# Optimization experiments

Measured on AMD Instinct MI355X. Metric: run time of the kernel, lower is better.

## Reference

```python
import jax, jax.numpy as jnp
import numpy as np

B, A = 8192, 16
HID, NK, NQ, NV = 256, 32, 32, 128
IN_DIM, CUR_HID, CUR_OUT, N_ACT = 512, 512, 128, 64
EXT_LAMBD, INT_LAMBD = 1.0, 0.5


def setup_inputs() -> dict:
    key = jax.random.key(0)
    ks = jax.random.split(key, 16)
    def w(k, i, o):
        return jax.random.normal(k, (i, o), jnp.float32) / np.sqrt(i)
    return {
        'x': jax.random.normal(ks[0], (B * A, IN_DIM), jnp.float32),
        'hidden': jax.random.normal(ks[1], (B, A, HID), jnp.float32),
        'Wk': w(ks[2], HID, NK), 'bk': jnp.zeros((NK,), jnp.float32),
        'Wv': w(ks[3], HID, NV), 'bv': jnp.zeros((NV,), jnp.float32),
        'Wq': w(ks[4], HID, NQ), 'bq': jnp.zeros((NQ,), jnp.float32),
        'Wa': w(ks[5], NQ + NK * A, A), 'ba': jnp.zeros((A,), jnp.float32),
        'Wt1': w(ks[6], IN_DIM, CUR_HID), 'bt1': jnp.zeros((CUR_HID,), jnp.float32),
        'Wt2': w(ks[7], CUR_HID, CUR_OUT), 'bt2': jnp.zeros((CUR_OUT,), jnp.float32),
        'Wp1': w(ks[8], IN_DIM, CUR_HID), 'bp1': jnp.zeros((CUR_HID,), jnp.float32),
        'Wp2': w(ks[9], CUR_HID, CUR_HID), 'bp2': jnp.zeros((CUR_HID,), jnp.float32),
        'Wp3': w(ks[10], CUR_HID, CUR_OUT), 'bp3': jnp.zeros((CUR_OUT,), jnp.float32),
        'Wc': w(ks[11], NV + HID, HID), 'bc': jnp.zeros((HID,), jnp.float32),
        'W2': w(ks[12], HID, N_ACT), 'b2': jnp.zeros((N_ACT,), jnp.float32),
    }


def _aggregate(x, hidden, Wk, bk, Wv, bv, Wq, bq, Wa, ba, Wt1, bt1, Wt2, bt2,
               Wp1, bp1, Wp2, bp2, Wp3, bp3, Wc, bc, W2, b2):
    # communicate(): per-agent key / value / query projections
    key_ = hidden @ Wk + bk          # [B, A, NK]
    value = hidden @ Wv + bv         # [B, A, NV]
    query = hidden @ Wq + bq         # [B, A, NQ]
    # torch.cat([key[:, i, :] for i in range(A)], -1) == reshape; repeat == broadcast
    flat_key = key_.reshape(B, A * NK)
    qk = jnp.concatenate(
        [query, jnp.broadcast_to(flat_key[:, None, :], (B, A, A * NK))], axis=-1)
    attn_weights = jax.nn.softmax(qk @ Wa + ba, axis=-1)   # [B, A, A]
    # intrinsic-motivation predictors (dropout p=0.5 in eval mode -> identity)
    tar = jax.nn.relu(x @ Wt1 + bt1) @ Wt2 + bt2           # [B*A, CUR_OUT]
    pred = jax.nn.relu(x @ Wp1 + bp1)
    pred = jax.nn.relu(pred @ Wp2 + bp2)
    pred = pred @ Wp3 + bp3
    int_imp = jnp.mean((tar - pred) ** 2, axis=-1).reshape(B, A)
    int_imp = jax.nn.softmax(int_imp, axis=-1)             # [B, A]
    # view(B,A,1).repeat(1,1,A).permute(0,2,1): out[b,i,j] = int_imp[b,j]
    int_mat = jnp.broadcast_to(int_imp[:, None, :], (B, A, A))
    attn = EXT_LAMBD * attn_weights + INT_LAMBD * jax.lax.stop_gradient(int_mat)
    applied = jnp.einsum('bij,bjv->biv', attn, value)      # [B, A, NV]
    comb = jax.nn.relu(jnp.concatenate([applied, hidden], axis=-1) @ Wc + bc)
    return comb @ W2 + b2                                  # [B, A, N_ACT]


def reference(x, hidden, Wk, bk, Wv, bv, Wq, bq, Wa, ba, Wt1, bt1, Wt2, bt2,
              Wp1, bp1, Wp2, bp2, Wp3, bp3, Wc, bc, W2, b2):
    return _aggregate(x, hidden, Wk, bk, Wv, bv, Wq, bq, Wa, ba, Wt1, bt1,
                      Wt2, bt2, Wp1, bp1, Wp2, bp2, Wp3, bp3, Wc, bc, W2, b2)
```

## Files before the change

### kernel.cpp

```cpp
#include <hip/hip_runtime.h>
#include <cstddef>
#include <cstdint>

typedef unsigned short ushort_t;
typedef __attribute__((ext_vector_type(4))) float f32x4;
typedef __attribute__((ext_vector_type(8))) short bf16x8;

#define BB   8192
#define AA   16
#define BA   131072

__device__ __forceinline__ float bf2f(ushort_t u) {
    union { float f; uint32_t i; } v; v.i = ((uint32_t)u) << 16; return v.f;
}
__device__ __forceinline__ ushort_t f2bf(float f) {
    union { float f; uint32_t i; } v; v.f = f;
    uint32_t r = v.i + 0x7fffu + ((v.i >> 16) & 1u);
    return (ushort_t)(r >> 16);
}
__device__ __forceinline__ void gload_lds16(const void* g, void* l) {
    __builtin_amdgcn_global_load_lds(
        (const __attribute__((address_space(1))) uint32_t*)g,
        (__attribute__((address_space(3))) uint32_t*)l, 16, 0, 0);
}

template<bool RELU, bool FUSE_OUT>
__global__ __launch_bounds__(512, 2)
void gemm8p(const ushort_t* __restrict__ A, int lda,
            const ushort_t* __restrict__ A2, int lda2, int ksplit,
            const ushort_t* __restrict__ Bt,
            const float* __restrict__ bias,
            ushort_t* __restrict__ C, int ldc, int K, int lgx, int rpx,
            const ushort_t* __restrict__ W2t, const float* __restrict__ b2)
{
    __shared__ ushort_t lds[65536];

    const int tid  = threadIdx.x;
    const int w    = tid >> 6;
    const int lane = tid & 63;
    const int wm   = w >> 2;
    const int wn   = w & 3;
    const int fr   = lane & 15;
    const int fq   = lane >> 4;

    const int bid  = blockIdx.x;
    const int xcd  = bid & 7;
    const int slot = bid >> 3;
    const int x    = slot & ((1 << lgx) - 1);
    const int y    = xcd * rpx + (slot >> lgx);
    const size_t brow = (size_t)y * 256;
    const int    bcol = x * 256;

    const int NT = K >> 6;
    const int NI = NT >> 1;

    const int srl = tid >> 3;
    const int spg = tid & 7;

    f32x4 acc[8][4];
#pragma unroll
    for (int m = 0; m < 8; ++m)
#pragma unroll
        for (int n = 0; n < 4; ++n) acc[m][n] = (f32x4){0.f, 0.f, 0.f, 0.f};

    const ushort_t* aB1[4];
    const ushort_t* aB2[4];
    const ushort_t* bB[4];
    int ldsA[4], ldsB[4];
#pragma unroll
    for (int s = 0; s < 4; ++s) {
        const int rowA = (srl < 32) ? s * 32 + srl : 128 + s * 32 + (srl - 32);
        const int colA = ((spg ^ (rowA & 7)) << 3);
        aB1[s] = A  + (brow + rowA) * (size_t)lda  + colA;
        aB2[s] = A2 + (brow + rowA) * (size_t)lda2 + colA - ksplit;
        ldsA[s] = rowA * 64 + spg * 8;
        const int rowB = s * 64 + srl;
        const int colB = ((spg ^ (rowB & 7)) << 3);
        bB[s]   = Bt + (size_t)(bcol + rowB) * K + colB;
        ldsB[s] = 16384 + rowB * 64 + spg * 8;
    }

    auto stageA = [&](int T, int s, int bi) {
        const int k0 = T << 6;
        const ushort_t* src = (k0 >= ksplit ? aB2[s] : aB1[s]) + k0;
        gload_lds16(src, &lds[(bi << 15) + ldsA[s]]);
    };
    auto stageB = [&](int T, int c, int bi) {
        gload_lds16(bB[c] + (T << 6), &lds[(bi << 15) + ldsB[c]]);
    };

    stageA(0, 0, 0); stageB(0, 0, 0);
    stageA(0, 1, 0); stageB(0, 1, 0);
    stageA(0, 2, 0); stageB(0, 2, 0);
    stageA(0, 3, 0); stageB(0, 3, 0);
    stageA(1, 0, 1); stageB(1, 0, 1);
    stageA(1, 1, 1); stageB(1, 1, 1);
    stageA(1, 2, 1); stageB(1, 2, 1);

    bf16x8 breg[4][2];

    for (int i = 0; i < NI; ++i) {
        const bool more = (i + 1 < NI);
#pragma unroll
        for (int h = 0; h < 2; ++h) {
            const int bufA = h << 15;
            const int bufB = (h << 15) + 16384;
#pragma unroll
            for (int q = 0; q < 4; ++q) {
                if (q == 0) {
                    if (h == 0 || more) asm volatile("s_waitcnt vmcnt(6)" ::: "memory");
                    else                asm volatile("s_waitcnt vmcnt(0)" ::: "memory");
                    __builtin_amdgcn_sched_barrier(0);
                    __builtin_amdgcn_s_barrier();
#pragma unroll
                    for (int n = 0; n < 4; ++n)
#pragma unroll
                        for (int kk = 0; kk < 2; ++kk) {
                            const int row = wn * 64 + n * 16 + fr;
                            const int gp  = ((kk * 4 + fq) ^ (row & 7)) << 3;
                            breg[n][kk] = *(const bf16x8*)&lds[bufB + row * 64 + gp];
                        }
                }
                bf16x8 areg[2][2];
#pragma unroll
                for (int j = 0; j < 2; ++j)
#pragma unroll
                    for (int kk = 0; kk < 2; ++kk) {
                        const int row = wm * 128 + (2 * q + j) * 16 + fr;
                        const int gp  = ((kk * 4 + fq) ^ (row & 7)) << 3;
                        areg[j][kk] = *(const bf16x8*)&lds[bufA + row * 64 + gp];
                    }
                if (h == 0) {
                    if (q == 0)      { stageA(2*i+1, 3, 1); stageB(2*i+1, 3, 1); }
                    else if (more)   { stageA(2*i+2, q-1, 0); stageB(2*i+2, q-1, 0); }
                } else {
                    if (q == 0) { if (more) { stageA(2*i+2, 3, 0); stageB(2*i+2, 3, 0); } }
                    else        { if (more) { stageA(2*i+3, q-1, 1); stageB(2*i+3, q-1, 1); } }
                }
                __builtin_amdgcn_s_setprio(1);
#pragma unroll
                for (int j = 0; j < 2; ++j)
#pragma unroll
                    for (int n = 0; n < 4; ++n)
#pragma unroll
                        for (int kk = 0; kk < 2; ++kk)
                            acc[2*q+j][n] = __builtin_amdgcn_mfma_f32_16x16x32_bf16(
                                areg[j][kk], breg[n][kk], acc[2*q+j][n], 0, 0, 0);
                __builtin_amdgcn_s_setprio(0);
                __builtin_amdgcn_s_barrier();
            }
        }
    }

    if (!FUSE_OUT) {
#pragma unroll
        for (int m = 0; m < 8; ++m) {
            const size_t rowb = brow + wm * 128 + m * 16 + fq * 4;
#pragma unroll
            for (int n = 0; n < 4; ++n) {
                const int col = bcol + wn * 64 + n * 16 + fr;
                const float bv = bias[col];
#pragma unroll
                for (int r = 0; r < 4; ++r) {
                    float v = acc[m][n][r] + bv;
                    if (RELU) v = fmaxf(v, 0.f);
                    C[(rowb + r) * (size_t)ldc + col] = f2bf(v);
                }
            }
        }
    } else {
#pragma unroll
        for (int m = 0; m < 8; ++m) {
            const int row = wm * 128 + m * 16 + fq * 4;
#pragma unroll
            for (int n = 0; n < 4; ++n) {
                const int col = wn * 64 + n * 16 + fr;
                const float bv = bias[col];
#pragma unroll
                for (int r = 0; r < 4; ++r) {
                    const float v = fmaxf(acc[m][n][r] + bv, 0.f);
                    const int rr = row + r;
                    const int g  = (col >> 3) ^ (rr & 7);
                    lds[rr * 256 + g * 8 + (col & 7)] = f2bf(v);
                }
            }
        }
        bf16x8 w2f[4][8];
#pragma unroll
        for (int n2 = 0; n2 < 4; ++n2)
#pragma unroll
            for (int kk = 0; kk < 8; ++kk)
                w2f[n2][kk] = *(const bf16x8*)&W2t[(n2 * 16 + fr) * 256 + kk * 32 + fq * 8];
        __syncthreads();
        f32x4 acc2[2][4];
#pragma unroll
        for (int m2 = 0; m2 < 2; ++m2)
#pragma unroll
            for (int n2 = 0; n2 < 4; ++n2) acc2[m2][n2] = (f32x4){0.f, 0.f, 0.f, 0.f};
#pragma unroll
        for (int kk = 0; kk < 8; ++kk) {
#pragma unroll
            for (int m2 = 0; m2 < 2; ++m2) {
                const int row = w * 32 + m2 * 16 + fr;
                const int g   = (kk * 4 + fq) ^ (row & 7);
                const bf16x8 af = *(const bf16x8*)&lds[row * 256 + g * 8];
#pragma unroll
                for (int n2 = 0; n2 < 4; ++n2)
                    acc2[m2][n2] = __builtin_amdgcn_mfma_f32_16x16x32_bf16(
                        af, w2f[n2][kk], acc2[m2][n2], 0, 0, 0);
            }
        }
        float* outp = (float*)C;
#pragma unroll
        for (int m2 = 0; m2 < 2; ++m2) {
            const size_t rowb = brow + w * 32 + m2 * 16 + fq * 4;
#pragma unroll
            for (int n2 = 0; n2 < 4; ++n2) {
                const int col = n2 * 16 + fr;
                const float bv = b2[col];
#pragma unroll
                for (int r = 0; r < 4; ++r)
                    outp[(rowb + r) * 64 + col] = acc2[m2][n2][r] + bv;
            }
        }
    }
}

template<bool OBF16, bool RELU, bool MSE>
__global__ __launch_bounds__(256)
void gemm_mfma(const ushort_t* __restrict__ A, int lda,
               const ushort_t* __restrict__ A2, int lda2, int ksplit,
               const ushort_t* __restrict__ Bt,
               const float* __restrict__ bias,
               void* __restrict__ C, int ldc, int N, int K, int lgx,
               float* __restrict__ iimp_out)
{
    __shared__ ushort_t As[2][128 * 64];
    __shared__ ushort_t Bs[2][128 * 64];

    const int tid  = threadIdx.x;
    const int w    = tid >> 6;
    const int lane = tid & 63;
    const int wm   = w >> 1;
    const int wn   = w & 1;

    const int bid  = blockIdx.x;
    const int xcd  = bid & 7;
    const int slot = bid >> 3;
    const int x    = slot & ((1 << lgx) - 1);
    const int y    = xcd * 128 + (slot >> lgx);
    const size_t brow = (size_t)y * 128;
    const int    bcol = x * 128;

    const int fr   = lane & 15;
    const int fq   = lane >> 4;
    const int srow = lane >> 3;
    const int scol = (lane & 7) << 3;

    f32x4 acc[4][4];
#pragma unroll
    for (int i = 0; i < 4; ++i)
#pragma unroll
        for (int j = 0; j < 4; ++j) acc[i][j] = (f32x4){0.f, 0.f, 0.f, 0.f};

    const int NT = K >> 6;

    auto stage = [&](int buf, int k0) {
#pragma unroll
        for (int i = 0; i < 4; ++i) {
            const int c = (w << 2) + i;
            const int r = (c << 3) + srow;
            const ushort_t* asrc;
            if (k0 >= ksplit)
                asrc = A2 + (brow + r) * (size_t)lda2 + (k0 - ksplit) + scol;
            else
                asrc = A  + (brow + r) * (size_t)lda  + k0 + scol;
            gload_lds16(asrc, &As[buf][(c << 9) + lane * 8]);
            gload_lds16(Bt + (size_t)(bcol + r) * K + k0 + scol,
                        &Bs[buf][(c << 9) + lane * 8]);
        }
    };

    stage(0, 0);
    __syncthreads();

    for (int t = 0; t < NT; ++t) {
        const int cur = t & 1;
        if (t + 1 < NT) stage(cur ^ 1, (t + 1) << 6);
#pragma unroll
        for (int kk = 0; kk < 2; ++kk) {
            bf16x8 a[4], b[4];
#pragma unroll
            for (int f = 0; f < 4; ++f) {
                a[f] = *(const bf16x8*)&As[cur][(wm * 64 + f * 16 + fr) * 64 + kk * 32 + fq * 8];
                b[f] = *(const bf16x8*)&Bs[cur][(wn * 64 + f * 16 + fr) * 64 + kk * 32 + fq * 8];
            }
#pragma unroll
            for (int fm = 0; fm < 4; ++fm)
#pragma unroll
                for (int fn = 0; fn < 4; ++fn)
                    acc[fm][fn] = __builtin_amdgcn_mfma_f32_16x16x32_bf16(
                        a[fm], b[fn], acc[fm][fn], 0, 0, 0);
        }
        __syncthreads();
    }

    if (MSE) {
        float* rowsq = (float*)As;
        if (tid < 128) rowsq[tid] = 0.f;
        __syncthreads();
#pragma unroll
        for (int fm = 0; fm < 4; ++fm) {
#pragma unroll
            for (int r = 0; r < 4; ++r) {
                float s = 0.f;
#pragma unroll
                for (int fn = 0; fn < 4; ++fn) {
                    const int col = wn * 64 + fn * 16 + fr;
                    const float v = acc[fm][fn][r] + bias[col];
                    s += v * v;
                }
                s += __shfl_xor(s, 1);
                s += __shfl_xor(s, 2);
                s += __shfl_xor(s, 4);
                s += __shfl_xor(s, 8);
                if (fr == 0)
                    atomicAdd(&rowsq[wm * 64 + fm * 16 + fq * 4 + r], s);
            }
        }
        __syncthreads();
        if (tid < 8) {
            const int rb = tid * 16;
            float mv[16], mx = -1e30f;
#pragma unroll
            for (int a = 0; a < 16; ++a) {
                mv[a] = rowsq[rb + a] * (1.f / 128.f);
                mx = fmaxf(mx, mv[a]);
            }
            float e[16], den = 0.f;
#pragma unroll
            for (int a = 0; a < 16; ++a) { e[a] = __expf(mv[a] - mx); den += e[a]; }
            const float inv = 1.f / den;
            const size_t b = brow / 16 + tid;
#pragma unroll
            for (int a = 0; a < 16; ++a) iimp_out[b * 16 + a] = e[a] * inv;
        }
        return;
    }

#pragma unroll
    for (int fm = 0; fm < 4; ++fm) {
        const size_t rowb = brow + wm * 64 + fm * 16 + fq * 4;
#pragma unroll
        for (int fn = 0; fn < 4; ++fn) {
            const int col = bcol + wn * 64 + fn * 16 + fr;
            if (col < N) {
                const float bv = bias[col];
#pragma unroll
                for (int r = 0; r < 4; ++r) {
                    float v = acc[fm][fn][r] + bv;
                    if (RELU) v = fmaxf(v, 0.f);
                    const size_t idx = (rowb + r) * (size_t)ldc + col;
                    if (OBF16) ((ushort_t*)C)[idx] = f2bf(v);
                    else       ((float*)C)[idx]    = v;
                }
            }
        }
    }
}

__global__ __launch_bounds__(256)
void transpose_w(const float* __restrict__ W, ushort_t* __restrict__ Wt,
                 int K, int N, int Npad)
{
    int idx = blockIdx.x * 256 + threadIdx.x;
    if (idx >= Npad * K) return;
    int n = idx / K, k = idx - n * K;
    float v = (n < N) ? W[(size_t)k * N + n] : 0.f;
    Wt[idx] = f2bf(v);
}

__global__ __launch_bounds__(256)
void transpose_wk(const float* __restrict__ W, ushort_t* __restrict__ Wt,
                  int Ksrc, int N, int ldk, int kOff, float sign)
{
    int idx = blockIdx.x * 256 + threadIdx.x;
    if (idx >= N * Ksrc) return;
    int n = idx / Ksrc, k = idx - n * Ksrc;
    Wt[(size_t)n * ldk + kOff + k] = f2bf(sign * W[(size_t)k * N + n]);
}

__global__ __launch_bounds__(256)
void conv_f32_bf16(const float* __restrict__ src, ushort_t* __restrict__ dst)
{
    size_t q = (size_t)blockIdx.x * 256 + threadIdx.x;
    float4 v = ((const float4*)src)[q];
    ushort_t* d = dst + q * 4;
    d[0] = f2bf(v.x); d[1] = f2bf(v.y); d[2] = f2bf(v.z); d[3] = f2bf(v.w);
}

__global__ void pack_cat2(const float* __restrict__ a, const float* __restrict__ b,
                          float* __restrict__ o)
{
    int j = blockIdx.x * 256 + threadIdx.x;
    if (j < 512) o[j] = a[j];
    else if (j < 1024) o[j] = b[j - 512];
}

__global__ void pack_bias(const float* __restrict__ bk, const float* __restrict__ bq,
                          const float* __restrict__ bv, float* __restrict__ pb)
{
    int j = threadIdx.x;
    float v = 0.f;
    if      (j < 32)  v = bk[j];
    else if (j < 64)  v = bq[j - 32];
    else if (j < 192) v = bv[j - 64];
    pb[j] = v;
}

__global__ void make_cbias(const float* __restrict__ bt2, const float* __restrict__ bp3,
                           float* __restrict__ cb)
{
    int j = threadIdx.x;
    cb[j] = bt2[j] - bp3[j];
}

__global__ __launch_bounds__(256)
void attn_apply(const ushort_t* __restrict__ kvq, const float* __restrict__ Wa,
                const float* __restrict__ ba, const float* __restrict__ iimp,
                ushort_t* __restrict__ applied)
{
    const int b = blockIdx.x, t = threadIdx.x;
    __shared__ float klds[512], qlds[512];
    __shared__ ushort_t vlds[2048];
    __shared__ float part[16][17];
    __shared__ float kp[16];
    __shared__ float attn[16][17];

    for (int i = t; i < 512; i += 256) {
        int a = i >> 5, c = i & 31;
        const size_t base = ((size_t)b * AA + a) * 192;
        klds[i] = bf2f(kvq[base + c]);
        qlds[i] = bf2f(kvq[base + 32 + c]);
    }
    for (int i = t; i < 2048; i += 256) {
        int j = i >> 7, v = i & 127;
        vlds[i] = kvq[((size_t)b * AA + j) * 192 + 64 + v];
    }
    __syncthreads();

    {
        int j = t & 15, seg = t >> 4;
        float s = 0.f;
        for (int c = seg * 32; c < seg * 32 + 32; ++c)
            s += klds[c] * Wa[(32 + c) * 16 + j];
        part[j][seg] = s;
    }
    __syncthreads();
    if (t < 16) {
        float s = 0.f;
#pragma unroll
        for (int seg = 0; seg < 16; ++seg) s += part[t][seg];
        kp[t] = s;
    }
    __syncthreads();

    {
        int i = t >> 4, j = t & 15;
        float s = 0.f;
#pragma unroll
        for (int q = 0; q < 32; ++q) s += qlds[i * 32 + q] * Wa[q * 16 + j];
        attn[i][j] = s + kp[j] + ba[j];
    }
    __syncthreads();
    if (t < 16) {
        float mx = -1e30f;
#pragma unroll
        for (int j = 0; j < 16; ++j) mx = fmaxf(mx, attn[t][j]);
        float e[16], den = 0.f;
#pragma unroll
        for (int j = 0; j < 16; ++j) { e[j] = __expf(attn[t][j] - mx); den += e[j]; }
        float inv = 1.f / den;
#pragma unroll
        for (int j = 0; j < 16; ++j)
            attn[t][j] = e[j] * inv + 0.5f * iimp[b * 16 + j];
    }
    __syncthreads();

    for (int o = t; o < 2048; o += 256) {
        int i = o >> 7, v = o & 127;
        float s = 0.f;
#pragma unroll
        for (int j = 0; j < 16; ++j) s += attn[i][j] * bf2f(vlds[j * 128 + v]);
        applied[((size_t)b * AA + i) * 128 + v] = f2bf(s);
    }
}

extern "C" void kernel_launch(void* const* d_in, const int* in_sizes, int n_in,
                              void* d_out, int out_size, void* d_ws, size_t ws_size,
                              hipStream_t stream)
{
    const float* x      = (const float*)d_in[0];
    const float* hidden = (const float*)d_in[1];
    const float* Wk  = (const float*)d_in[2];
    const float* bk  = (const float*)d_in[3];
    const float* Wv  = (const float*)d_in[4];
    const float* bv  = (const float*)d_in[5];
    const float* Wq  = (const float*)d_in[6];
    const float* bq  = (const float*)d_in[7];
    const float* Wa  = (const float*)d_in[8];
    const float* ba  = (const float*)d_in[9];
    const float* Wt1 = (const float*)d_in[10];
    const float* bt1 = (const float*)d_in[11];
    const float* Wt2 = (const float*)d_in[12];
    const float* bt2 = (const float*)d_in[13];
    const float* Wp1 = (const float*)d_in[14];
    const float* bp1 = (const float*)d_in[15];
    const float* Wp2 = (const float*)d_in[16];
    const float* bp2 = (const float*)d_in[17];
    const float* Wp3 = (const float*)d_in[18];
    const float* bp3 = (const float*)d_in[19];
    const float* Wc  = (const float*)d_in[20];
    const float* bc  = (const float*)d_in[21];
    const float* W2  = (const float*)d_in[22];
    const float* b2  = (const float*)d_in[23];

    float*    out = (float*)d_out;
    ushort_t* ws  = (ushort_t*)d_ws;

    ushort_t* xb  = ws;
    ushort_t* ht2 = xb + (size_t)BA * 512;
    ushort_t* hp2 = ht2 + (size_t)BA * 1024;
    ushort_t* WT  = hp2 + (size_t)BA * 512;
    ushort_t* kvq     = xb;
    ushort_t* hiddenb = hp2;
    ushort_t* applied = ht2;

    ushort_t* Bg1  = WT;
    ushort_t* Wp2t = Bg1  + 1024 * 512;
    ushort_t* Dt   = Wp2t + 512 * 512;
    ushort_t* Wkvq = Dt   + 128 * 1024;
    ushort_t* Wct  = Wkvq + 256 * 256;
    ushort_t* W2t  = Wct  + 256 * 384;
    float* g1bias = (float*)(W2t + 128 * 256);
    float* pbias  = g1bias + 1024;
    float* cbias  = pbias + 256;
    float* iimp   = cbias + 128;

    const dim3 blk(256);
    const int BIG = 1 << 30;

    transpose_w<<<1024, blk, 0, stream>>>(Wt1, Bg1,             512, 512, 512);
    transpose_w<<<1024, blk, 0, stream>>>(Wp1, Bg1 + 512 * 512, 512, 512, 512);
    transpose_w<<<1024, blk, 0, stream>>>(Wp2, Wp2t, 512, 512, 512);
    transpose_wk<<<256, blk, 0, stream>>>(Wt2, Dt, 512, 128, 1024, 0,    1.f);
    transpose_wk<<<256, blk, 0, stream>>>(Wp3, Dt, 512, 128, 1024, 512, -1.f);
    transpose_w<<<32,  blk, 0, stream>>>(Wk, Wkvq + 0 * 256,   256, 32, 32);
    transpose_w<<<32,  blk, 0, stream>>>(Wq, Wkvq + 32 * 256,  256, 32, 32);
    transpose_w<<<128, blk, 0, stream>>>(Wv, Wkvq + 64 * 256,  256, 128, 128);
    transpose_w<<<64,  blk, 0, stream>>>(Wk, Wkvq + 192 * 256, 256, 0, 64);
    transpose_w<<<384, blk, 0, stream>>>(Wc, Wct, 384, 256, 256);
    transpose_w<<<128, blk, 0, stream>>>(W2, W2t, 256, 64, 128);
    pack_cat2<<<4, 256, 0, stream>>>(bt1, bp1, g1bias);
    pack_bias<<<1, 256, 0, stream>>>(bk, bq, bv, pbias);
    make_cbias<<<1, 128, 0, stream>>>(bt2, bp3, cbias);

    conv_f32_bf16<<<65536, blk, 0, stream>>>(x, xb);
    gemm8p<true, false><<<2048, 512, 0, stream>>>(
        xb, 512, xb, 512, BIG, Bg1, g1bias, ht2, 1024, 512, 2, 64, nullptr, nullptr);
    gemm8p<true, false><<<1024, 512, 0, stream>>>(
        ht2 + 512, 1024, ht2 + 512, 1024, BIG, Wp2t, bp2, hp2, 512, 512, 1, 64, nullptr, nullptr);
    gemm_mfma<true, false, true><<<1024, blk, 0, stream>>>(
        ht2, 1024, hp2, 512, 512, Dt, cbias, nullptr, 128, 128, 1024, 0, iimp);

    conv_f32_bf16<<<32768, blk, 0, stream>>>(hidden, hiddenb);
    gemm_mfma<true, false, false><<<2048, blk, 0, stream>>>(
        hiddenb, 256, hiddenb, 256, BIG, Wkvq, pbias, kvq, 192, 192, 256, 1, nullptr);
    attn_apply<<<BB, blk, 0, stream>>>(kvq, Wa, ba, iimp, applied);

    gemm8p<true, true><<<512, 512, 0, stream>>>(
        applied, 128, hiddenb, 256, 128, Wct, bc, (ushort_t*)out, 64, 384, 0, 64, W2t, b2);
}
```

Measured before the change: 599.7 us.

## Run curiosity predictor MLP GEMMs in FP8 e4m3 instead of bf16

Converts x and the curiosity-network weights (Wt1, Wp1, Wp2, Wt2, Wp3) to FP8 e4m3. It adds new FP8 MFMA GEMM kernels, including a swizzled-LDS 256x256 tile version and an FP8 MSE+softmax reduction kernel, and the intermediate activations are stored as FP8. The aim is to halve memory traffic and double matrix throughput for the dominant 131072x512 GEMMs. The risk is accuracy: intermediate activations and the tar-pred difference are quantized to 3-bit mantissa with no scaling. The attention and output paths stay in bf16, and the workspace layout is reorganized to fit.

```diff
diff --git a/kernel.cpp b/kernel.cpp
--- a/kernel.cpp
+++ b/kernel.cpp
@@ -3,6 +3,7 @@
 #include <cstdint>
 
 typedef unsigned short ushort_t;
+typedef unsigned char  u8_t;
 typedef __attribute__((ext_vector_type(4))) float f32x4;
 typedef __attribute__((ext_vector_type(8))) short bf16x8;
 
@@ -18,10 +19,274 @@
     uint32_t r = v.i + 0x7fffu + ((v.i >> 16) & 1u);
     return (ushort_t)(r >> 16);
 }
+__device__ __forceinline__ u8_t f2e4m3(float f) {
+    union { float f; uint32_t u; } v; v.f = f;
+    uint32_t s = (v.u >> 24) & 0x80u;
+    float a = fabsf(f);
+    if (a >= 448.f) return (u8_t)(s | 0x7Eu);
+    union { float f; uint32_t u; } w; w.f = a;
+    int E = (int)(w.u >> 23) - 127;
+    if (E < -6) E = -6;
+    union { uint32_t u; float f; } qs; qs.u = (uint32_t)(127 + 3 - E) << 23;
+    int m = (int)rintf(a * qs.f);
+    if (m >= 16) { m >>= 1; ++E; if (E > 8) return (u8_t)(s | 0x7Eu); }
+    if (m >= 8)  return (u8_t)(s | ((uint32_t)(E + 7) << 3) | (uint32_t)(m - 8));
+    return (u8_t)(s | (uint32_t)m);
+}
 __device__ __forceinline__ void gload_lds16(const void* g, void* l) {
     __builtin_amdgcn_global_load_lds(
         (const __attribute__((address_space(1))) uint32_t*)g,
         (__attribute__((address_space(3))) uint32_t*)l, 16, 0, 0);
+}
+
+template<bool RELU>
+__global__ __launch_bounds__(512, 2)
+void gemm8p_fp8(const u8_t* __restrict__ A, int lda,
+                const u8_t* __restrict__ A2, int lda2, int ksplit,
+                const u8_t* __restrict__ Bt,
+                const float* __restrict__ bias,
+                u8_t* __restrict__ C, int ldc, int K, int lgx, int rpx)
+{
+    __shared__ u8_t lds[65536];
+
+    const int tid  = threadIdx.x;
+    const int w    = tid >> 6;
+    const int lane = tid & 63;
+    const int wm   = w >> 2;
+    const int wn   = w & 3;
+    const int fr   = lane & 15;
+    const int fq   = lane >> 4;
+
+    const int bid  = blockIdx.x;
+    const int xcd  = bid & 7;
+    const int slot = bid >> 3;
+    const int x    = slot & ((1 << lgx) - 1);
+    const int y    = xcd * rpx + (slot >> lgx);
+    const size_t brow = (size_t)y * 256;
+    const int    bcol = x * 256;
+
+    const int NT = K >> 6;
+
+    f32x4 acc[8][4];
+#pragma unroll
+    for (int m = 0; m < 8; ++m)
+#pragma unroll
+        for (int n = 0; n < 4; ++n) acc[m][n] = (f32x4){0.f, 0.f, 0.f, 0.f};
+
+    size_t aoff[2], a2off[2], boff[2];
+    int aldso[2], bldso[2];
+#pragma unroll
+    for (int j = 0; j < 2; ++j) {
+        const int r = tid + (j << 9);
+        const int l = r >> 3;
+        const int p = r & 7;
+        const int g = p ^ (l & 7);
+        const int row  = 2 * l + (g >> 2);
+        const int colb = (g & 3) * 16;
+        aoff[j]  = (brow + row) * (size_t)lda  + colb;
+        a2off[j] = (brow + row) * (size_t)lda2 + colb;
+        boff[j]  = (size_t)(bcol + row) * K + colb;
+        aldso[j] = r * 16;
+        bldso[j] = 16384 + r * 16;
+    }
+
+    auto stage_tile = [&](int T) {
+        const int k0   = T << 6;
+        const int base = (T & 1) << 15;
+        const bool hi  = (k0 >= ksplit);
+#pragma unroll
+        for (int j = 0; j < 2; ++j) {
+            const u8_t* src = hi ? (A2 + a2off[j] + (k0 - ksplit))
+                                 : (A  + aoff[j]  + k0);
+            gload_lds16(src, &lds[base + aldso[j]]);
+        }
+#pragma unroll
+        for (int j = 0; j < 2; ++j)
+            gload_lds16(Bt + boff[j] + k0, &lds[base + bldso[j]]);
+    };
+
+    stage_tile(0);
+
+    unsigned long breg[4][2];
+
+    for (int t = 0; t < NT; ++t) {
+        const int base = (t & 1) << 15;
+#pragma unroll
+        for (int q = 0; q < 4; ++q) {
+            if (q == 0) {
+                asm volatile("s_waitcnt vmcnt(0)" ::: "memory");
+                __builtin_amdgcn_sched_barrier(0);
+                __builtin_amdgcn_s_barrier();
+#pragma unroll
+                for (int n = 0; n < 4; ++n)
+#pragma unroll
+                    for (int kk = 0; kk < 2; ++kk) {
+                        const int row  = wn * 64 + n * 16 + fr;
+                        const int l    = row >> 1;
+                        const int slotq = kk * 2 + (fq >> 1);
+                        const int g    = (row & 1) * 4 + slotq;
+                        const int p    = g ^ (l & 7);
+                        const int addr = base + 16384 + l * 128 + p * 16 + (fq & 1) * 8;
+                        breg[n][kk] = *(const unsigned long*)&lds[addr];
+                    }
+                if (t + 1 < NT) stage_tile(t + 1);
+            }
+            unsigned long areg[2][2];
+#pragma unroll
+            for (int j = 0; j < 2; ++j)
+#pragma unroll
+                for (int kk = 0; kk < 2; ++kk) {
+                    const int row  = wm * 128 + (2 * q + j) * 16 + fr;
+                    const int l    = row >> 1;
+                    const int slotq = kk * 2 + (fq >> 1);
+                    const int g    = (row & 1) * 4 + slotq;
+                    const int p    = g ^ (l & 7);
+                    const int addr = base + l * 128 + p * 16 + (fq & 1) * 8;
+                    areg[j][kk] = *(const unsigned long*)&lds[addr];
+                }
+            __builtin_amdgcn_s_setprio(1);
+#pragma unroll
+            for (int j = 0; j < 2; ++j)
+#pragma unroll
+                for (int n = 0; n < 4; ++n)
+#pragma unroll
+                    for (int kk = 0; kk < 2; ++kk)
+                        acc[2*q+j][n] = __builtin_amdgcn_mfma_f32_16x16x32_fp8_fp8(
+                            (long)areg[j][kk], (long)breg[n][kk], acc[2*q+j][n], 0, 0, 0);
+            __builtin_amdgcn_s_setprio(0);
+            __builtin_amdgcn_s_barrier();
+        }
+    }
+
+#pragma unroll
+    for (int m = 0; m < 8; ++m) {
+        const size_t rowb = brow + wm * 128 + m * 16 + fq * 4;
+#pragma unroll
+        for (int n = 0; n < 4; ++n) {
+            const int col = bcol + wn * 64 + n * 16 + fr;
+            const float bv = bias[col];
+#pragma unroll
+            for (int r = 0; r < 4; ++r) {
+                float v = acc[m][n][r] + bv;
+                if (RELU) v = fmaxf(v, 0.f);
+                C[(rowb + r) * (size_t)ldc + col] = f2e4m3(v);
+            }
+        }
+    }
+}
+
+__global__ __launch_bounds__(256)
+void gemm_mfma_fp8_mse(const u8_t* __restrict__ A, int lda,
+                       const u8_t* __restrict__ A2, int lda2, int ksplit,
+                       const u8_t* __restrict__ Bt,
+                       const float* __restrict__ bias,
+                       int K, float* __restrict__ iimp_out)
+{
+    __shared__ u8_t As[2][8192];
+    __shared__ u8_t Bs[2][8192];
+
+    const int tid  = threadIdx.x;
+    const int w    = tid >> 6;
+    const int lane = tid & 63;
+    const int wm   = w >> 1;
+    const int wn   = w & 1;
+
+    const int bid  = blockIdx.x;
+    const int xcd  = bid & 7;
+    const int slot = bid >> 3;
+    const int y    = xcd * 128 + slot;
+    const size_t brow = (size_t)y * 128;
+
+    const int fr = lane & 15;
+    const int fq = lane >> 4;
+
+    f32x4 acc[4][4];
+#pragma unroll
+    for (int i = 0; i < 4; ++i)
+#pragma unroll
+        for (int j = 0; j < 4; ++j) acc[i][j] = (f32x4){0.f, 0.f, 0.f, 0.f};
+
+    const int NT = K >> 6;
+
+    auto stage = [&](int buf, int k0) {
+#pragma unroll
+        for (int j = 0; j < 2; ++j) {
+            const int gi  = tid + (j << 8);
+            const int row = gi >> 2;
+            const int cb  = (gi & 3) * 16;
+            const u8_t* asrc;
+            if (k0 >= ksplit)
+                asrc = A2 + (brow + row) * (size_t)lda2 + (k0 - ksplit) + cb;
+            else
+                asrc = A  + (brow + row) * (size_t)lda  + k0 + cb;
+            gload_lds16(asrc, &As[buf][gi * 16]);
+            gload_lds16(Bt + (size_t)row * K + k0 + cb, &Bs[buf][gi * 16]);
+        }
+    };
+
+    stage(0, 0);
+    __syncthreads();
+
+    for (int t = 0; t < NT; ++t) {
+        const int cur = t & 1;
+        if (t + 1 < NT) stage(cur ^ 1, (t + 1) << 6);
+#pragma unroll
+        for (int kk = 0; kk < 2; ++kk) {
+            unsigned long a[4], b[4];
+#pragma unroll
+            for (int f = 0; f < 4; ++f) {
+                a[f] = *(const unsigned long*)&As[cur][(wm * 64 + f * 16 + fr) * 64 + kk * 32 + fq * 8];
+                b[f] = *(const unsigned long*)&Bs[cur][(wn * 64 + f * 16 + fr) * 64 + kk * 32 + fq * 8];
+            }
+#pragma unroll
+            for (int fm = 0; fm < 4; ++fm)
+#pragma unroll
+                for (int fn = 0; fn < 4; ++fn)
+                    acc[fm][fn] = __builtin_amdgcn_mfma_f32_16x16x32_fp8_fp8(
+                        (long)a[fm], (long)b[fn], acc[fm][fn], 0, 0, 0);
+        }
+        __syncthreads();
+    }
+
+    float* rowsq = (float*)As;
+    if (tid < 128) rowsq[tid] = 0.f;
+    __syncthreads();
+#pragma unroll
+    for (int fm = 0; fm < 4; ++fm) {
+#pragma unroll
+        for (int r = 0; r < 4; ++r) {
+            float s = 0.f;
+#pragma unroll
+            for (int fn = 0; fn < 4; ++fn) {
+                const int col = wn * 64 + fn * 16 + fr;
+                const float v = acc[fm][fn][r] + bias[col];
+                s += v * v;
+            }
+            s += __shfl_xor(s, 1);
+            s += __shfl_xor(s, 2);
+            s += __shfl_xor(s, 4);
+            s += __shfl_xor(s, 8);
+            if (fr == 0)
+                atomicAdd(&rowsq[wm * 64 + fm * 16 + fq * 4 + r], s);
+        }
+    }
+    __syncthreads();
+    if (tid < 8) {
+        const int rb = tid * 16;
+        float mv[16], mx = -1e30f;
+#pragma unroll
+        for (int a = 0; a < 16; ++a) {
+            mv[a] = rowsq[rb + a] * (1.f / 128.f);
+            mx = fmaxf(mx, mv[a]);
+        }
+        float e[16], den = 0.f;
+#pragma unroll
+        for (int a = 0; a < 16; ++a) { e[a] = __expf(mv[a] - mx); den += e[a]; }
+        const float inv = 1.f / den;
+        const size_t b = brow / 16 + tid;
+#pragma unroll
+        for (int a = 0; a < 16; ++a) iimp_out[b * 16 + a] = e[a] * inv;
+    }
 }
 
 template<bool RELU, bool FUSE_OUT>
@@ -226,14 +491,11 @@
     }
 }
 
-template<bool OBF16, bool RELU, bool MSE>
 __global__ __launch_bounds__(256)
 void gemm_mfma(const ushort_t* __restrict__ A, int lda,
-               const ushort_t* __restrict__ A2, int lda2, int ksplit,
                const ushort_t* __restrict__ Bt,
                const float* __restrict__ bias,
-               void* __restrict__ C, int ldc, int N, int K, int lgx,
-               float* __restrict__ iimp_out)
+               ushort_t* __restrict__ C, int ldc, int N, int K, int lgx)
 {
     __shared__ ushort_t As[2][128 * 64];
     __shared__ ushort_t Bs[2][128 * 64];
@@ -270,12 +532,8 @@
         for (int i = 0; i < 4; ++i) {
             const int c = (w << 2) + i;
             const int r = (c << 3) + srow;
-            const ushort_t* asrc;
-            if (k0 >= ksplit)
-                asrc = A2 + (brow + r) * (size_t)lda2 + (k0 - ksplit) + scol;
-            else
-                asrc = A  + (brow + r) * (size_t)lda  + k0 + scol;
-            gload_lds16(asrc, &As[buf][(c << 9) + lane * 8]);
+            gload_lds16(A + (brow + r) * (size_t)lda + k0 + scol,
+                        &As[buf][(c << 9) + lane * 8]);
             gload_lds16(Bt + (size_t)(bcol + r) * K + k0 + scol,
                         &Bs[buf][(c << 9) + lane * 8]);
         }
@@ -303,49 +561,6 @@
                         a[fm], b[fn], acc[fm][fn], 0, 0, 0);
         }
         __syncthreads();
-    }
-
-    if (MSE) {
-        float* rowsq = (float*)As;
-        if (tid < 128) rowsq[tid] = 0.f;
-        __syncthreads();
-#pragma unroll
-        for (int fm = 0; fm < 4; ++fm) {
-#pragma unroll
-            for (int r = 0; r < 4; ++r) {
-                float s = 0.f;
-#pragma unroll
-                for (int fn = 0; fn < 4; ++fn) {
-                    const int col = wn * 64 + fn * 16 + fr;
-                    const float v = acc[fm][fn][r] + bias[col];
-                    s += v * v;
-                }
-                s += __shfl_xor(s, 1);
-                s += __shfl_xor(s, 2);
-                s += __shfl_xor(s, 4);
-                s += __shfl_xor(s, 8);
-                if (fr == 0)
-                    atomicAdd(&rowsq[wm * 64 + fm * 16 + fq * 4 + r], s);
-            }
-        }
-        __syncthreads();
-        if (tid < 8) {
-            const int rb = tid * 16;
-            float mv[16], mx = -1e30f;
-#pragma unroll
-            for (int a = 0; a < 16; ++a) {
-                mv[a] = rowsq[rb + a] * (1.f / 128.f);
-                mx = fmaxf(mx, mv[a]);
-            }
-            float e[16], den = 0.f;
-#pragma unroll
-            for (int a = 0; a < 16; ++a) { e[a] = __expf(mv[a] - mx); den += e[a]; }
-            const float inv = 1.f / den;
-            const size_t b = brow / 16 + tid;
-#pragma unroll
-            for (int a = 0; a < 16; ++a) iimp_out[b * 16 + a] = e[a] * inv;
-        }
-        return;
     }
 
 #pragma unroll
@@ -357,13 +572,8 @@
             if (col < N) {
                 const float bv = bias[col];
 #pragma unroll
-                for (int r = 0; r < 4; ++r) {
-                    float v = acc[fm][fn][r] + bv;
-                    if (RELU) v = fmaxf(v, 0.f);
-                    const size_t idx = (rowb + r) * (size_t)ldc + col;
-                    if (OBF16) ((ushort_t*)C)[idx] = f2bf(v);
-                    else       ((float*)C)[idx]    = v;
-                }
+                for (int r = 0; r < 4; ++r)
+                    C[(rowb + r) * (size_t)ldc + col] = f2bf(acc[fm][fn][r] + bv);
             }
         }
     }
@@ -381,13 +591,24 @@
 }
 
 __global__ __launch_bounds__(256)
-void transpose_wk(const float* __restrict__ W, ushort_t* __restrict__ Wt,
-                  int Ksrc, int N, int ldk, int kOff, float sign)
+void transpose_w_fp8(const float* __restrict__ W, u8_t* __restrict__ Wt,
+                     int K, int N, int Npad)
+{
+    int idx = blockIdx.x * 256 + threadIdx.x;
+    if (idx >= Npad * K) return;
+    int n = idx / K, k = idx - n * K;
+    float v = (n < N) ? W[(size_t)k * N + n] : 0.f;
+    Wt[idx] = f2e4m3(v);
+}
+
+__global__ __launch_bounds__(256)
+void transpose_wk_fp8(const float* __restrict__ W, u8_t* __restrict__ Wt,
+                      int Ksrc, int N, int ldk, int kOff, float sign)
 {
     int idx = blockIdx.x * 256 + threadIdx.x;
     if (idx >= N * Ksrc) return;
     int n = idx / Ksrc, k = idx - n * Ksrc;
-    Wt[(size_t)n * ldk + kOff + k] = f2bf(sign * W[(size_t)k * N + n]);
+    Wt[(size_t)n * ldk + kOff + k] = f2e4m3(sign * W[(size_t)k * N + n]);
 }
 
 __global__ __launch_bounds__(256)
@@ -397,6 +618,16 @@
     float4 v = ((const float4*)src)[q];
     ushort_t* d = dst + q * 4;
     d[0] = f2bf(v.x); d[1] = f2bf(v.y); d[2] = f2bf(v.z); d[3] = f2bf(v.w);
+}
+
+__global__ __launch_bounds__(256)
+void conv_f32_fp8(const float* __restrict__ src, u8_t* __restrict__ dst)
+{
+    size_t q = (size_t)blockIdx.x * 256 + threadIdx.x;
+    float4 v = ((const float4*)src)[q];
+    uint32_t pk = (uint32_t)f2e4m3(v.x) | ((uint32_t)f2e4m3(v.y) << 8) |
+                  ((uint32_t)f2e4m3(v.z) << 16) | ((uint32_t)f2e4m3(v.w) << 24);
+    ((uint32_t*)dst)[q] = pk;
 }
 
 __global__ void pack_cat2(const float* __restrict__ a, const float* __restrict__ b,
@@ -525,21 +756,21 @@
     const float* W2  = (const float*)d_in[22];
     const float* b2  = (const float*)d_in[23];
 
-    float*    out = (float*)d_out;
-    ushort_t* ws  = (ushort_t*)d_ws;
-
-    ushort_t* xb  = ws;
-    ushort_t* ht2 = xb + (size_t)BA * 512;
-    ushort_t* hp2 = ht2 + (size_t)BA * 1024;
-    ushort_t* WT  = hp2 + (size_t)BA * 512;
-    ushort_t* kvq     = xb;
-    ushort_t* hiddenb = hp2;
-    ushort_t* applied = ht2;
-
-    ushort_t* Bg1  = WT;
-    ushort_t* Wp2t = Bg1  + 1024 * 512;
-    ushort_t* Dt   = Wp2t + 512 * 512;
-    ushort_t* Wkvq = Dt   + 128 * 1024;
+    float* out = (float*)d_out;
+    u8_t*  ws8 = (u8_t*)d_ws;
+
+    u8_t* xb8 = ws8;
+    u8_t* ht8 = xb8 + (size_t)BA * 512;
+    u8_t* hp8 = ht8 + (size_t)BA * 1024;
+    u8_t* WT  = hp8 + (size_t)BA * 512;
+    ushort_t* hiddenb = (ushort_t*)xb8;
+    ushort_t* kvq     = (ushort_t*)ht8;
+    ushort_t* applied = (ushort_t*)(ht8 + (size_t)BA * 384);
+
+    u8_t* Bg1   = WT;
+    u8_t* Wp2t8 = Bg1 + 1024 * 512;
+    u8_t* Dt8   = Wp2t8 + 512 * 512;
+    ushort_t* Wkvq = (ushort_t*)(Dt8 + 128 * 1024);
     ushort_t* Wct  = Wkvq + 256 * 256;
     ushort_t* W2t  = Wct  + 256 * 384;
     float* g1bias = (float*)(W2t + 128 * 256);
@@ -550,11 +781,11 @@
     const dim3 blk(256);
     const int BIG = 1 << 30;
 
-    transpose_w<<<1024, blk, 0, stream>>>(Wt1, Bg1,             512, 512, 512);
-    transpose_w<<<1024, blk, 0, stream>>>(Wp1, Bg1 + 512 * 512, 512, 512, 512);
-    transpose_w<<<1024, blk, 0, stream>>>(Wp2, Wp2t, 512, 512, 512);
-    transpose_wk<<<256, blk, 0, stream>>>(Wt2, Dt, 512, 128, 1024, 0,    1.f);
-    transpose_wk<<<256, blk, 0, stream>>>(Wp3, Dt, 512, 128, 1024, 512, -1.f);
+    transpose_w_fp8<<<1024, blk, 0, stream>>>(Wt1, Bg1,             512, 512, 512);
+    transpose_w_fp8<<<1024, blk, 0, stream>>>(Wp1, Bg1 + 512 * 512, 512, 512, 512);
+    transpose_w_fp8<<<1024, blk, 0, stream>>>(Wp2, Wp2t8, 512, 512, 512);
+    transpose_wk_fp8<<<256, blk, 0, stream>>>(Wt2, Dt8, 512, 128, 1024, 0,    1.f);
+    transpose_wk_fp8<<<256, blk, 0, stream>>>(Wp3, Dt8, 512, 128, 1024, 512, -1.f);
     transpose_w<<<32,  blk, 0, stream>>>(Wk, Wkvq + 0 * 256,   256, 32, 32);
     transpose_w<<<32,  blk, 0, stream>>>(Wq, Wkvq + 32 * 256,  256, 32, 32);
     transpose_w<<<128, blk, 0, stream>>>(Wv, Wkvq + 64 * 256,  256, 128, 128);
@@ -565,17 +796,17 @@
     pack_bias<<<1, 256, 0, stream>>>(bk, bq, bv, pbias);
     make_cbias<<<1, 128, 0, stream>>>(bt2, bp3, cbias);
 
-    conv_f32_bf16<<<65536, blk, 0, stream>>>(x, xb);
-    gemm8p<true, false><<<2048, 512, 0, stream>>>(
-        xb, 512, xb, 512, BIG, Bg1, g1bias, ht2, 1024, 512, 2, 64, nullptr, nullptr);
-    gemm8p<true, false><<<1024, 512, 0, stream>>>(
-        ht2 + 512, 1024, ht2 + 512, 1024, BIG, Wp2t, bp2, hp2, 512, 512, 1, 64, nullptr, nullptr);
-    gemm_mfma<true, false, true><<<1024, blk, 0, stream>>>(
-        ht2, 1024, hp2, 512, 512, Dt, cbias, nullptr, 128, 128, 1024, 0, iimp);
-
+    conv_f32_fp8<<<65536, blk, 0, stream>>>(x, xb8);
+    gemm8p_fp8<true><<<2048, 512, 0, stream>>>(
+        xb8, 512, xb8, 512, BIG, Bg1, g1bias, ht8, 1024, 512, 2, 64);
     conv_f32_bf16<<<32768, blk, 0, stream>>>(hidden, hiddenb);
-    gemm_mfma<true, false, false><<<2048, blk, 0, stream>>>(
-        hiddenb, 256, hiddenb, 256, BIG, Wkvq, pbias, kvq, 192, 192, 256, 1, nullptr);
+    gemm8p_fp8<true><<<1024, 512, 0, stream>>>(
+        ht8 + 512, 1024, ht8 + 512, 1024, BIG, Wp2t8, bp2, hp8, 512, 512, 1, 64);
+    gemm_mfma_fp8_mse<<<1024, blk, 0, stream>>>(
+        ht8, 1024, hp8, 512, 512, Dt8, cbias, 1024, iimp);
+
+    gemm_mfma<<<2048, blk, 0, stream>>>(
+        hiddenb, 256, Wkvq, pbias, kvq, 192, 192, 256, 1);
     attn_apply<<<BB, blk, 0, stream>>>(kvq, Wa, ba, iimp, applied);
 
     gemm8p<true, true><<<512, 512, 0, stream>>>(
```

Measured after the change: 781.7 us. +30.3%, slower.
